# Optimization experiments

Measured on AMD Instinct MI355X. Metric: run time of the kernel, lower is better.

Reference implementation:

```python
import jax, jax.numpy as jnp
import numpy as np

B, T, D, H = 4, 2048, 1024, 16
DH = D // H  # 64
EPS = 1e-5


def _layernorm(x, g, b):
    mu = jnp.mean(x, axis=-1, keepdims=True)
    var = jnp.var(x, axis=-1, keepdims=True)
    return (x - mu) * jax.lax.rsqrt(var + EPS) * g + b


def setup_inputs() -> dict:
    key = jax.random.key(0)
    ks = jax.random.split(key, 12)
    s = 0.02
    x = jax.random.normal(ks[0], (B, T, D), dtype=jnp.float32)
    # causal mask (the repo registers tril as the eos_mask buffer)
    eos_mask = jnp.broadcast_to(jnp.tril(jnp.ones((T, T), dtype=jnp.int32)), (B, T, T))
    Wq = jax.random.normal(ks[1], (H, D, DH), dtype=jnp.float32) * s
    Wk = jax.random.normal(ks[2], (H, D, DH), dtype=jnp.float32) * s
    Wv = jax.random.normal(ks[3], (H, D, DH), dtype=jnp.float32) * s
    Wp = jax.random.normal(ks[4], (D, D), dtype=jnp.float32) * s
    bp = jnp.zeros((D,), dtype=jnp.float32)
    W1 = jax.random.normal(ks[5], (D, 4 * D), dtype=jnp.float32) * s
    b1 = jnp.zeros((4 * D,), dtype=jnp.float32)
    W2 = jax.random.normal(ks[6], (4 * D, D), dtype=jnp.float32) * s
    b2 = jnp.zeros((D,), dtype=jnp.float32)
    g1 = jnp.ones((D,), dtype=jnp.float32)
    beta1 = jnp.zeros((D,), dtype=jnp.float32)
    g2 = jnp.ones((D,), dtype=jnp.float32)
    beta2 = jnp.zeros((D,), dtype=jnp.float32)
    return dict(x=x, eos_mask=eos_mask, Wq=Wq, Wk=Wk, Wv=Wv, Wp=Wp, bp=bp,
                W1=W1, b1=b1, W2=W2, b2=b2, g1=g1, beta1=beta1, g2=g2, beta2=beta2)


def reference(x, eos_mask, Wq, Wk, Wv, Wp, bp, W1, b1, W2, b2, g1, beta1, g2, beta2):
    # x: [B,T,D]; eos_mask: [B,T,T]
    x1 = _layernorm(x, g1, beta1)
    q = jnp.einsum('btd,hdk->bhtk', x1, Wq)
    k = jnp.einsum('btd,hdk->bhtk', x1, Wk)
    v = jnp.einsum('btd,hdk->bhtk', x1, Wv)
    # NOTE: original scales by 1/sqrt(C) where C = d_model (not d_head)
    scores = jnp.einsum('bhtk,bhsk->bhts', q, k) / np.sqrt(x.shape[-1]).astype(np.float32)
    scores = jnp.where(eos_mask[:, None, :, :] == 0, jnp.float32(-jnp.inf), scores)
    wei = jax.nn.softmax(scores, axis=-1)
    attn = jnp.einsum('bhts,bhsk->bhtk', wei, v)          # [B,H,T,DH]
    attn = attn.transpose(0, 2, 1, 3).reshape(x.shape)    # concat heads -> [B,T,D]
    attn = attn @ Wp + bp
    x2 = x1 + attn
    x3 = _layernorm(x2, g2, beta2)
    mlp = jax.nn.relu(x3 @ W1 + b1) @ W2 + b2
    out = x3 + mlp
    return out
```

## Files before the change

kernel.cpp:

```cpp
#include <hip/hip_runtime.h>


#define B_ 4
#define T_ 2048
#define D_ 1024
#define H_ 16
#define DH_ 64

using u16 = unsigned short;
typedef short bf16x8 __attribute__((ext_vector_type(8)));
typedef float f32x4 __attribute__((ext_vector_type(4)));

#define GLOAD_LDS16(g, l)                                                          \
  __builtin_amdgcn_global_load_lds((const __attribute__((address_space(1))) void*)(g), \
                                   (__attribute__((address_space(3))) void*)(l), 16, 0, 0)

#define CVTPK(d, lo, hi) asm("v_cvt_pk_bf16_f32 %0, %1, %2" : "=v"(d) : "v"(lo), "v"(hi))

__device__ __forceinline__ f32x4 mfma16(bf16x8 a, bf16x8 b, f32x4 c) {
  return __builtin_amdgcn_mfma_f32_16x16x32_bf16(a, b, c, 0, 0, 0);
}

__device__ __forceinline__ u16 f2bf(float f) {
  union { float f; unsigned u; } v; v.f = f;
  unsigned r = v.u + 0x7fffu + ((v.u >> 16) & 1u);
  return (u16)(r >> 16);
}
__device__ __forceinline__ float bf2f(u16 h) {
  union { unsigned u; float f; } v; v.u = ((unsigned)h) << 16; return v.f;
}

template<typename TI>
__global__ __launch_bounds__(256)
void ln_kernel(const TI* __restrict__ x, const float* __restrict__ g,
               const float* __restrict__ be, u16* __restrict__ yb)
{
  const int row = blockIdx.x;
  const int tid = threadIdx.x;
  float v0, v1, v2, v3;
  if constexpr (sizeof(TI) == 4) {
    const float4 vx = ((const float4*)(x + (size_t)row * D_))[tid];
    v0 = vx.x; v1 = vx.y; v2 = vx.z; v3 = vx.w;
  } else {
    const ushort4 vx = ((const ushort4*)((const u16*)x + (size_t)row * D_))[tid];
    v0 = bf2f(vx.x); v1 = bf2f(vx.y); v2 = bf2f(vx.z); v3 = bf2f(vx.w);
  }
  float s  = v0 + v1 + v2 + v3;
  float s2 = v0*v0 + v1*v1 + v2*v2 + v3*v3;
#pragma unroll
  for (int m = 1; m < 64; m <<= 1) { s += __shfl_xor(s, m); s2 += __shfl_xor(s2, m); }
  __shared__ float red[8];
  const int w = tid >> 6;
  if ((tid & 63) == 0) { red[w] = s; red[4 + w] = s2; }
  __syncthreads();
  s  = red[0] + red[1] + red[2] + red[3];
  s2 = red[4] + red[5] + red[6] + red[7];
  const float mu   = s * (1.0f / D_);
  const float rstd = rsqrtf(s2 * (1.0f / D_) - mu * mu + 1e-5f);
  const float4 gg = ((const float4*)g)[tid];
  const float4 bb = ((const float4*)be)[tid];
  ushort4 pk;
  pk.x = f2bf((v0 - mu) * rstd * gg.x + bb.x);
  pk.y = f2bf((v1 - mu) * rstd * gg.y + bb.y);
  pk.z = f2bf((v2 - mu) * rstd * gg.z + bb.z);
  pk.w = f2bf((v3 - mu) * rstd * gg.w + bb.w);
  ((ushort4*)(yb + (size_t)row * D_))[tid] = pk;
}

__global__ __launch_bounds__(256)
void transpose_cvt(const float* __restrict__ in, u16* __restrict__ out, int R, int C)
{
  __shared__ float tile[32][33];
  const int c0 = blockIdx.x * 32, r0 = blockIdx.y * 32;
  const float* ip = in + (size_t)blockIdx.z * R * C;
  u16* op = out + (size_t)blockIdx.z * R * C;
  const int tx = threadIdx.x, ty = threadIdx.y;
#pragma unroll
  for (int j = 0; j < 4; ++j)
    tile[ty + j * 8][tx] = ip[(size_t)(r0 + ty + j * 8) * C + (c0 + tx)];
  __syncthreads();
#pragma unroll
  for (int j = 0; j < 4; ++j)
    op[(size_t)(c0 + ty + j * 8) * R + (r0 + tx)] = f2bf(tile[tx][ty + j * 8]);
}

#define MODE_QKV 0
#define MODE_WP 1
#define MODE_MLP1 2
#define MODE_MLP2 3

template<int MODE>
__global__ __launch_bounds__(512, 4)
void gemm128(const u16* __restrict__ A, const u16* __restrict__ Bt,
             int M, int N, int K,
             const float* __restrict__ bias, const u16* __restrict__ resid,
             float* __restrict__ outf, u16* __restrict__ outb,
             u16* __restrict__ qo, u16* __restrict__ ko, u16* __restrict__ vo)
{
  __shared__ __align__(16) u16 Ash[2][128 * 64];
  __shared__ __align__(16) u16 Bsh[2][128 * 64];
  const int t = threadIdx.x, w = t >> 6, l = t & 63, lg = l >> 4, lr = l & 15;
  const int wr = w >> 2, wc = w & 3;

  const int gx = gridDim.x;
  const int nwg = gx * gridDim.y;
  const int bid = blockIdx.y * gx + blockIdx.x;
  const int cpx = nwg >> 3;
  const int virt = (bid & 7) * cpx + (bid >> 3);
  const int bn0 = (virt % gx) * 128, bm0 = (virt / gx) * 128;

  f32x4 acc[4][2] = {};

  const int srow = t >> 3;
  const int sc16 = (t & 7) ^ (srow & 7);
  const u16* gAs = A  + (size_t)(bm0 + srow) * K + sc16 * 8;
  const u16* gBs = Bt + (size_t)(bn0 + srow) * K + sc16 * 8;

#define ISS_A(R, BUF, ko) GLOAD_LDS16(gAs + (size_t)(R) * 64 * K + (ko), &Ash[BUF][(R) * 4096 + w * 512])
#define ISS_B(R, BUF, ko) GLOAD_LDS16(gBs + (size_t)(R) * 64 * K + (ko), &Bsh[BUF][(R) * 4096 + w * 512])

  ISS_A(0, 0, 0); ISS_A(1, 0, 0); ISS_B(0, 0, 0); ISS_B(1, 0, 0);
  ISS_A(0, 1, 64); ISS_A(1, 1, 64); ISS_B(0, 1, 64); ISS_B(1, 1, 64);

  auto rdA = [&](int buf, int m, int kk) -> bf16x8 {
    const int r = wr * 64 + m * 16 + lr;
    return *(const bf16x8*)((const char*)&Ash[buf][0] + r * 128 + (((kk * 4 + lg) ^ (r & 7)) << 4));
  };
  auto rdB = [&](int buf, int n, int kk) -> bf16x8 {
    const int r = wc * 32 + n * 16 + lr;
    return *(const bf16x8*)((const char*)&Bsh[buf][0] + r * 128 + (((kk * 4 + lg) ^ (r & 7)) << 4));
  };

  const int nkt = K >> 6;
  for (int i = 0; i < nkt; ++i) {
    const int buf = i & 1;
    if (i + 1 < nkt) asm volatile("s_waitcnt vmcnt(4)" ::: "memory");
    else             asm volatile("s_waitcnt vmcnt(0)" ::: "memory");
    __builtin_amdgcn_s_barrier();
    __builtin_amdgcn_sched_barrier(0);

    bf16x8 afr[4][2], bfr[2][2];
#pragma unroll
    for (int m = 0; m < 4; ++m) { afr[m][0] = rdA(buf, m, 0); afr[m][1] = rdA(buf, m, 1); }
#pragma unroll
    for (int n = 0; n < 2; ++n) { bfr[n][0] = rdB(buf, n, 0); bfr[n][1] = rdB(buf, n, 1); }

    __builtin_amdgcn_s_setprio(1);
#pragma unroll
    for (int m = 0; m < 4; ++m)
#pragma unroll
      for (int n = 0; n < 2; ++n) {
        acc[m][n] = mfma16(afr[m][0], bfr[n][0], acc[m][n]);
        acc[m][n] = mfma16(afr[m][1], bfr[n][1], acc[m][n]);
      }
    __builtin_amdgcn_s_setprio(0);
    __builtin_amdgcn_s_barrier();
    __builtin_amdgcn_sched_barrier(0);

    if (i + 2 < nkt) {
      const size_t ko = (size_t)(i + 2) << 6;
      ISS_A(0, buf, ko); ISS_A(1, buf, ko); ISS_B(0, buf, ko); ISS_B(1, buf, ko);
    }
  }
#undef ISS_A
#undef ISS_B

#pragma unroll
  for (int m = 0; m < 4; ++m) {
#pragma unroll
    for (int n = 0; n < 2; ++n) {
#pragma unroll
      for (int r = 0; r < 4; ++r) {
        const int row = bm0 + wr * 64 + m * 16 + lg * 4 + r;
        const int col = bn0 + wc * 32 + n * 16 + lr;
        float v = acc[m][n][r];
        if constexpr (MODE == MODE_QKV) {
          const int sel = col >> 10, hh = (col >> 6) & 15, dh = col & 63;
          const int bi = row >> 11, tt = row & 2047;
          u16* dst = (sel == 0) ? qo : (sel == 1) ? ko : vo;
          dst[(((size_t)bi * H_ + hh) * T_ + tt) * DH_ + dh] = f2bf(v);
        } else if constexpr (MODE == MODE_WP) {
          v += bias[col] + bf2f(resid[(size_t)row * N + col]);
          outb[(size_t)row * N + col] = f2bf(v);
        } else if constexpr (MODE == MODE_MLP1) {
          v += bias[col];
          outb[(size_t)row * N + col] = f2bf(v > 0.f ? v : 0.f);
        } else {
          outf[(size_t)row * N + col] = v + bias[col] + bf2f(resid[(size_t)row * N + col]);
        }
      }
    }
  }
}

__global__ __launch_bounds__(256, 2)
void attn_kernel(const u16* __restrict__ q, const u16* __restrict__ k,
                 const u16* __restrict__ v, u16* __restrict__ out)
{
  __shared__ __align__(16) u16 Ks[2][4096];
  __shared__ __align__(16) u16 Vt[2][4096];
  const int t = threadIdx.x, w = t >> 6, l = t & 63, lg = l >> 4, lr = l & 15;

  const int bid = blockIdx.x;
  const int virt = (bid & 7) * 256 + (bid >> 3);
  const int bh = (virt >> 8) * 8 + (virt & 7);
  const int qt = 31 - ((virt >> 3) & 31);

  const int b = bh >> 4, h = bh & 15;
  const u16* Qp = q + (size_t)bh * T_ * DH_;
  const u16* Kp = k + (size_t)bh * T_ * DH_;
  const u16* Vp = v + (size_t)bh * T_ * DH_;

  const int qrow = qt * 64 + w * 16 + lr;
  const bf16x8 qf0 = *(const bf16x8*)&Qp[(size_t)qrow * DH_ + lg * 8];
  const bf16x8 qf1 = *(const bf16x8*)&Qp[(size_t)qrow * DH_ + 32 + lg * 8];

  const int srow = t >> 3;
  const int kcol = (((t & 7) ^ (srow & 7)) << 3);
  const int vdh0 = (t & 7) << 3;
  const u16* Kg = Kp + (size_t)srow * DH_ + kcol;
  const u16* Vg = Vp + (size_t)srow * DH_ + vdh0;

  float m_run = -1e30f, l_run = 0.f;
  f32x4 o[4] = {};
  const float SC2 = 0.03125f * 1.44269504f;
  const float THR2 = 11.5416f;

  auto writeV = [&](int buf, uint4 va, uint4 vb) {
    const u16* pa = (const u16*)&va;
    const u16* pb = (const u16*)&vb;
    char* base = (char*)&Vt[buf][0];
#pragma unroll
    for (int j = 0; j < 8; ++j) {
      const int dh = vdh0 + j;
      const int swz = (((dh & 7) ^ ((dh >> 3) & 7)) << 4);
      *(u16*)(base + (((dh << 7) + (srow << 1)) ^ swz)) = pa[j];
      *(u16*)(base + (((dh << 7) + ((32 + srow) << 1)) ^ swz)) = pb[j];
    }
  };

  GLOAD_LDS16(Kg,            &Ks[0][w * 512]);
  GLOAD_LDS16(Kg + 32 * DH_, &Ks[0][2048 + w * 512]);
  {
    uint4 v0 = *(const uint4*)Vg;
    uint4 v1 = *(const uint4*)(Vg + 32 * DH_);
    writeV(0, v0, v1);
  }
  __syncthreads();

  const int nst = qt + 1;
  for (int st = 0; st < nst; ++st) {
    const int cur = st & 1, nxt = cur ^ 1;
    uint4 vA, vB;
    const bool pf = (st + 1 < nst);
    if (pf) {
      const u16* kg = Kg + (size_t)(st + 1) * 64 * DH_;
      GLOAD_LDS16(kg,            &Ks[nxt][w * 512]);
      GLOAD_LDS16(kg + 32 * DH_, &Ks[nxt][2048 + w * 512]);
      vA = *(const uint4*)(Vg + (size_t)(st + 1) * 64 * DH_);
      vB = *(const uint4*)(Vg + (size_t)(st + 1) * 64 * DH_ + 32 * DH_);
    }

    f32x4 sa[4] = {};
    const char* kb = (const char*)&Ks[cur][0];
    __builtin_amdgcn_s_setprio(1);
#pragma unroll
    for (int n = 0; n < 4; ++n) {
      const int sr = n * 16 + lr;
      const int base = (sr << 7) + (lg << 4);
      const int swz = (sr & 7) << 4;
      const bf16x8 b0 = *(const bf16x8*)(kb + (base ^ swz));
      const bf16x8 b1 = *(const bf16x8*)(kb + ((base + 64) ^ swz));
      sa[n] = mfma16(b0, qf0, sa[n]);
      sa[n] = mfma16(b1, qf1, sa[n]);
    }
    __builtin_amdgcn_s_setprio(0);

    float sc[4][4];
    float rm = -1e30f;
#pragma unroll
    for (int n = 0; n < 4; ++n)
#pragma unroll
      for (int r = 0; r < 4; ++r) {
        float x = sa[n][r] * SC2;
        if (st == qt && (st * 64 + n * 16 + lg * 4 + r) > qrow) x = -1e30f;
        sc[n][r] = x;
        rm = fmaxf(rm, x);
      }
    rm = fmaxf(rm, __shfl_xor(rm, 16));
    rm = fmaxf(rm, __shfl_xor(rm, 32));
    const bool noresc = __all(rm <= m_run + THR2);
    if (!noresc) {
      const float mnew = fmaxf(m_run, rm);
      const float al = exp2f(m_run - mnew);
      m_run = mnew;
      l_run *= al;
      const float alr0 = __shfl(al, lg * 4 + 0);
      const float alr1 = __shfl(al, lg * 4 + 1);
      const float alr2 = __shfl(al, lg * 4 + 2);
      const float alr3 = __shfl(al, lg * 4 + 3);
#pragma unroll
      for (int n = 0; n < 4; ++n) {
        o[n][0] *= alr0; o[n][1] *= alr1; o[n][2] *= alr2; o[n][3] *= alr3;
      }
    }
    float p[4][4];
    float rs = 0.f;
#pragma unroll
    for (int n = 0; n < 4; ++n)
#pragma unroll
      for (int r = 0; r < 4; ++r) {
        p[n][r] = exp2f(sc[n][r] - m_run);
        rs += p[n][r];
      }
    rs += __shfl_xor(rs, 16);
    rs += __shfl_xor(rs, 32);
    l_run += rs;

    unsigned pk0a, pk0b, pk1a, pk1b, pk2a, pk2b, pk3a, pk3b;
    CVTPK(pk0a, p[0][0], p[0][1]); CVTPK(pk0b, p[0][2], p[0][3]);
    CVTPK(pk1a, p[1][0], p[1][1]); CVTPK(pk1b, p[1][2], p[1][3]);
    CVTPK(pk2a, p[2][0], p[2][1]); CVTPK(pk2b, p[2][2], p[2][3]);
    CVTPK(pk3a, p[3][0], p[3][1]); CVTPK(pk3b, p[3][2], p[3][3]);

    const int srcA = lr + ((l >> 4) & 1) * 32;
    const int srcB = srcA + 16;
    const bool hi = (l >> 5) & 1;
    union { uint4 u; bf16x8 v8; } f0, f1;
    {
      const unsigned xA0 = __shfl(pk0a, srcA), xA1 = __shfl(pk0b, srcA);
      const unsigned yA0 = __shfl(pk1a, srcA), yA1 = __shfl(pk1b, srcA);
      const unsigned xB0 = __shfl(pk0a, srcB), xB1 = __shfl(pk0b, srcB);
      const unsigned yB0 = __shfl(pk1a, srcB), yB1 = __shfl(pk1b, srcB);
      f0.u.x = hi ? yA0 : xA0; f0.u.y = hi ? yA1 : xA1;
      f0.u.z = hi ? yB0 : xB0; f0.u.w = hi ? yB1 : xB1;
    }
    {
      const unsigned xA0 = __shfl(pk2a, srcA), xA1 = __shfl(pk2b, srcA);
      const unsigned yA0 = __shfl(pk3a, srcA), yA1 = __shfl(pk3b, srcA);
      const unsigned xB0 = __shfl(pk2a, srcB), xB1 = __shfl(pk2b, srcB);
      const unsigned yB0 = __shfl(pk3a, srcB), yB1 = __shfl(pk3b, srcB);
      f1.u.x = hi ? yA0 : xA0; f1.u.y = hi ? yA1 : xA1;
      f1.u.z = hi ? yB0 : xB0; f1.u.w = hi ? yB1 : xB1;
    }

    const char* vbase = (const char*)&Vt[cur][0];
    __builtin_amdgcn_s_setprio(1);
#pragma unroll
    for (int ks = 0; ks < 2; ++ks) {
      const bf16x8 pa = ks ? f1.v8 : f0.v8;
#pragma unroll
      for (int n = 0; n < 4; ++n) {
        const int dh = n * 16 + lr;
        int vbyte = (dh << 7) + (ks << 6) + (lg << 4);
        vbyte ^= (((dh & 7) ^ ((dh >> 3) & 7)) << 4);
        const bf16x8 vbf = *(const bf16x8*)(vbase + vbyte);
        o[n] = mfma16(pa, vbf, o[n]);
      }
    }
    __builtin_amdgcn_s_setprio(0);

    if (pf) writeV(nxt, vA, vB);
    __syncthreads();
  }

  const size_t obase = ((size_t)b * T_) * D_ + (size_t)h * DH_;
  float li[4];
  li[0] = 1.0f / __shfl(l_run, lg * 4 + 0);
  li[1] = 1.0f / __shfl(l_run, lg * 4 + 1);
  li[2] = 1.0f / __shfl(l_run, lg * 4 + 2);
  li[3] = 1.0f / __shfl(l_run, lg * 4 + 3);
#pragma unroll
  for (int n = 0; n < 4; ++n) {
#pragma unroll
    for (int r = 0; r < 4; ++r) {
      const int qg = qt * 64 + w * 16 + lg * 4 + r;
      out[obase + (size_t)qg * D_ + n * 16 + lr] = f2bf(o[n][r] * li[r]);
    }
  }
}

extern "C" void kernel_launch(void* const* d_in, const int* in_sizes, int n_in,
                              void* d_out, int out_size, void* d_ws, size_t ws_size,
                              hipStream_t stream) {
  (void)in_sizes; (void)n_in; (void)out_size; (void)ws_size;
  const float* x   = (const float*)d_in[0];
  const float* Wq  = (const float*)d_in[2];
  const float* Wk  = (const float*)d_in[3];
  const float* Wv  = (const float*)d_in[4];
  const float* Wp  = (const float*)d_in[5];
  const float* bp  = (const float*)d_in[6];
  const float* W1  = (const float*)d_in[7];
  const float* b1  = (const float*)d_in[8];
  const float* W2  = (const float*)d_in[9];
  const float* b2  = (const float*)d_in[10];
  const float* g1  = (const float*)d_in[11];
  const float* be1 = (const float*)d_in[12];
  const float* g2  = (const float*)d_in[13];
  const float* be2 = (const float*)d_in[14];

  char* ws = (char*)d_ws;
  const size_t MB16 = 16777216;
  u16* x1b   = (u16*)(ws);
  u16* qb    = (u16*)(ws + 1 * MB16);
  u16* kb    = (u16*)(ws + 2 * MB16);
  u16* vb    = (u16*)(ws + 3 * MB16);
  u16* attnb = (u16*)(ws + 4 * MB16);
  u16* x2b   = (u16*)(ws + 5 * MB16);
  u16* hb    = (u16*)(ws + 6 * MB16);
  u16* wqkvb = (u16*)(ws + 10 * MB16);
  u16* wpb   = (u16*)(ws + 10 * MB16 + 6291456);
  u16* w1b   = (u16*)(ws + 10 * MB16 + 8388608);
  u16* w2b   = (u16*)(ws + 11 * MB16);
  u16* x3b   = qb;

  dim3 tb(32, 8, 1);
  transpose_cvt<<<dim3(2, 32, 16),  tb, 0, stream>>>(Wq, wqkvb,                    1024, 64);
  transpose_cvt<<<dim3(2, 32, 16),  tb, 0, stream>>>(Wk, wqkvb + (size_t)1048576,  1024, 64);
  transpose_cvt<<<dim3(2, 32, 16),  tb, 0, stream>>>(Wv, wqkvb + (size_t)2097152,  1024, 64);
  transpose_cvt<<<dim3(32, 32, 1),  tb, 0, stream>>>(Wp, wpb, 1024, 1024);
  transpose_cvt<<<dim3(128, 32, 1), tb, 0, stream>>>(W1, w1b, 1024, 4096);
  transpose_cvt<<<dim3(32, 128, 1), tb, 0, stream>>>(W2, w2b, 4096, 1024);

  ln_kernel<float><<<8192, 256, 0, stream>>>(x, g1, be1, x1b);

  gemm128<MODE_QKV><<<dim3(24, 64), 512, 0, stream>>>(
      x1b, wqkvb, 8192, 3072, 1024, nullptr, nullptr, nullptr, nullptr, qb, kb, vb);

  attn_kernel<<<dim3(2048), 256, 0, stream>>>(qb, kb, vb, attnb);

  gemm128<MODE_WP><<<dim3(8, 64), 512, 0, stream>>>(
      attnb, wpb, 8192, 1024, 1024, bp, x1b, nullptr, x2b, nullptr, nullptr, nullptr);

  ln_kernel<u16><<<8192, 256, 0, stream>>>(x2b, g2, be2, x3b);

  gemm128<MODE_MLP1><<<dim3(32, 64), 512, 0, stream>>>(
      x3b, w1b, 8192, 4096, 1024, b1, nullptr, nullptr, hb, nullptr, nullptr, nullptr);

  gemm128<MODE_MLP2><<<dim3(8, 64), 512, 0, stream>>>(
      hb, w2b, 8192, 1024, 4096, b2, x3b, (float*)d_out, nullptr, nullptr, nullptr, nullptr);
}
```

Measured before the change: 378.5 us.

## Add 256x256-tile GEMM with interleaved load/compute phases for QKV and MLP1

Adds a new GEMM kernel with 256x256 output tiles per 512-thread workgroup. Each K-step is split into four compute phases, and the global-to-LDS loads for the next tile are interleaved between them. The QKV and MLP1 projections now use it instead of the 128x128 kernel. The aim is better operand reuse per byte loaded and better overlap of memory with MFMA work. In exchange it uses more LDS and registers per workgroup, and launches fewer workgroups (384 for QKV, 512 for MLP1), which may leave the GPU's CUs less evenly loaded.

```diff
diff --git a/kernel.cpp b/kernel.cpp
--- a/kernel.cpp
+++ b/kernel.cpp
@@ -16,6 +16,7 @@
                                    (__attribute__((address_space(3))) void*)(l), 16, 0, 0)
 
 #define CVTPK(d, lo, hi) asm("v_cvt_pk_bf16_f32 %0, %1, %2" : "=v"(d) : "v"(lo), "v"(hi))
+#define BARSB() do { __builtin_amdgcn_s_barrier(); __builtin_amdgcn_sched_barrier(0); } while (0)
 
 __device__ __forceinline__ f32x4 mfma16(bf16x8 a, bf16x8 b, f32x4 c) {
   return __builtin_amdgcn_mfma_f32_16x16x32_bf16(a, b, c, 0, 0, 0);
@@ -90,6 +91,159 @@
 #define MODE_MLP2 3
 
 template<int MODE>
+__global__ __launch_bounds__(512, 2)
+void gemm256v2(const u16* __restrict__ A, const u16* __restrict__ Bt,
+               int M, int N, int K,
+               const float* __restrict__ bias, const u16* __restrict__ resid,
+               float* __restrict__ outf, u16* __restrict__ outb,
+               u16* __restrict__ qo, u16* __restrict__ ko, u16* __restrict__ vo)
+{
+  __shared__ __align__(16) u16 Ash[2][256 * 64];
+  __shared__ __align__(16) u16 Bsh[2][256 * 64];
+  const int t = threadIdx.x, w = t >> 6, l = t & 63, lg = l >> 4, lr = l & 15;
+  const int wr = w >> 2, wc = w & 3;
+
+  const int gx = gridDim.x;
+  const int nwg = gx * gridDim.y;
+  const int bid = blockIdx.y * gx + blockIdx.x;
+  const int cpx = nwg >> 3;
+  const int virt = (bid & 7) * cpx + (bid >> 3);
+  const int bn0 = (virt % gx) * 256, bm0 = (virt / gx) * 256;
+
+  f32x4 acc[8][4] = {};
+
+  const int srow = t >> 3;
+  const int sc16 = (t & 7) ^ (srow & 7);
+  const u16* gAs = A  + (size_t)(bm0 + srow) * K + sc16 * 8;
+  const u16* gBs = Bt + (size_t)(bn0 + srow) * K + sc16 * 8;
+
+#define ISS2_A(R, BUF, ko) GLOAD_LDS16(gAs + (size_t)(R) * 64 * K + (ko), &Ash[BUF][(R) * 4096 + w * 512])
+#define ISS2_B(R, BUF, ko) GLOAD_LDS16(gBs + (size_t)(R) * 64 * K + (ko), &Bsh[BUF][(R) * 4096 + w * 512])
+
+  const int nkt = K >> 6;
+  ISS2_A(0, 0, 0); ISS2_A(1, 0, 0); ISS2_A(2, 0, 0); ISS2_A(3, 0, 0);
+  ISS2_B(0, 0, 0); ISS2_B(1, 0, 0); ISS2_B(2, 0, 0); ISS2_B(3, 0, 0);
+  if (nkt > 1) {
+    ISS2_A(0, 1, 64); ISS2_A(1, 1, 64);
+    asm volatile("s_waitcnt vmcnt(2)" ::: "memory");
+  } else {
+    asm volatile("s_waitcnt vmcnt(0)" ::: "memory");
+  }
+  BARSB();
+
+  auto rdA = [&](int buf, int m) -> bf16x8 {
+    const int r = wr * 128 + m * 16 + lr;
+    return *(const bf16x8*)((const char*)&Ash[buf][0] + r * 128 + (((0 + lg) ^ (r & 7)) << 4));
+  };
+  auto rdA1 = [&](int buf, int m) -> bf16x8 {
+    const int r = wr * 128 + m * 16 + lr;
+    return *(const bf16x8*)((const char*)&Ash[buf][0] + r * 128 + (((4 + lg) ^ (r & 7)) << 4));
+  };
+  auto rdB0 = [&](int buf, int n) -> bf16x8 {
+    const int r = wc * 64 + n * 16 + lr;
+    return *(const bf16x8*)((const char*)&Bsh[buf][0] + r * 128 + (((0 + lg) ^ (r & 7)) << 4));
+  };
+  auto rdB1 = [&](int buf, int n) -> bf16x8 {
+    const int r = wc * 64 + n * 16 + lr;
+    return *(const bf16x8*)((const char*)&Bsh[buf][0] + r * 128 + (((4 + lg) ^ (r & 7)) << 4));
+  };
+
+  bf16x8 afr[4][2], bfr[4][2];
+
+  for (int i = 0; i < nkt; ++i) {
+    const int buf = i & 1, nb = buf ^ 1;
+    const size_t k1 = (size_t)(i + 1) << 6, k2 = (size_t)(i + 2) << 6;
+    const bool n1 = (i + 1 < nkt), n2 = (i + 2 < nkt);
+
+#pragma unroll
+    for (int m = 0; m < 4; ++m) { afr[m][0] = rdA(buf, m); afr[m][1] = rdA1(buf, m); }
+#pragma unroll
+    for (int n = 0; n < 2; ++n) { bfr[n][0] = rdB0(buf, n); bfr[n][1] = rdB1(buf, n); }
+    if (n1) { ISS2_A(2, nb, k1); ISS2_A(3, nb, k1); }
+    BARSB();
+    __builtin_amdgcn_s_setprio(1);
+#pragma unroll
+    for (int m = 0; m < 4; ++m)
+#pragma unroll
+      for (int n = 0; n < 2; ++n) {
+        acc[m][n] = mfma16(afr[m][0], bfr[n][0], acc[m][n]);
+        acc[m][n] = mfma16(afr[m][1], bfr[n][1], acc[m][n]);
+      }
+    __builtin_amdgcn_s_setprio(0);
+    BARSB();
+
+#pragma unroll
+    for (int n = 2; n < 4; ++n) { bfr[n][0] = rdB0(buf, n); bfr[n][1] = rdB1(buf, n); }
+    if (n1) { ISS2_B(0, nb, k1); ISS2_B(1, nb, k1); }
+    BARSB();
+    __builtin_amdgcn_s_setprio(1);
+#pragma unroll
+    for (int m = 0; m < 4; ++m)
+#pragma unroll
+      for (int n = 2; n < 4; ++n) {
+        acc[m][n] = mfma16(afr[m][0], bfr[n][0], acc[m][n]);
+        acc[m][n] = mfma16(afr[m][1], bfr[n][1], acc[m][n]);
+      }
+    __builtin_amdgcn_s_setprio(0);
+    BARSB();
+
+#pragma unroll
+    for (int m = 0; m < 4; ++m) { afr[m][0] = rdA(buf, 4 + m); afr[m][1] = rdA1(buf, 4 + m); }
+    if (n1) { ISS2_B(2, nb, k1); ISS2_B(3, nb, k1); }
+    BARSB();
+    __builtin_amdgcn_s_setprio(1);
+#pragma unroll
+    for (int m = 0; m < 4; ++m)
+#pragma unroll
+      for (int n = 0; n < 2; ++n) {
+        acc[4 + m][n] = mfma16(afr[m][0], bfr[n][0], acc[4 + m][n]);
+        acc[4 + m][n] = mfma16(afr[m][1], bfr[n][1], acc[4 + m][n]);
+      }
+    __builtin_amdgcn_s_setprio(0);
+    BARSB();
+
+    if (n2) { ISS2_A(0, buf, k2); ISS2_A(1, buf, k2); }
+    BARSB();
+    __builtin_amdgcn_s_setprio(1);
+#pragma unroll
+    for (int m = 0; m < 4; ++m)
+#pragma unroll
+      for (int n = 2; n < 4; ++n) {
+        acc[4 + m][n] = mfma16(afr[m][0], bfr[n][0], acc[4 + m][n]);
+        acc[4 + m][n] = mfma16(afr[m][1], bfr[n][1], acc[4 + m][n]);
+      }
+    __builtin_amdgcn_s_setprio(0);
+    if (n2) asm volatile("s_waitcnt vmcnt(2)" ::: "memory");
+    else    asm volatile("s_waitcnt vmcnt(0)" ::: "memory");
+    BARSB();
+  }
+#undef ISS2_A
+#undef ISS2_B
+
+#pragma unroll
+  for (int m = 0; m < 8; ++m) {
+#pragma unroll
+    for (int n = 0; n < 4; ++n) {
+#pragma unroll
+      for (int r = 0; r < 4; ++r) {
+        const int row = bm0 + wr * 128 + m * 16 + lg * 4 + r;
+        const int col = bn0 + wc * 64 + n * 16 + lr;
+        float v = acc[m][n][r];
+        if constexpr (MODE == MODE_QKV) {
+          const int sel = col >> 10, hh = (col >> 6) & 15, dh = col & 63;
+          const int bi = row >> 11, tt = row & 2047;
+          u16* dst = (sel == 0) ? qo : (sel == 1) ? ko : vo;
+          dst[(((size_t)bi * H_ + hh) * T_ + tt) * DH_ + dh] = f2bf(v);
+        } else if constexpr (MODE == MODE_MLP1) {
+          v += bias[col];
+          outb[(size_t)row * N + col] = f2bf(v > 0.f ? v : 0.f);
+        }
+      }
+    }
+  }
+}
+
+template<int MODE>
 __global__ __launch_bounds__(512, 4)
 void gemm128(const u16* __restrict__ A, const u16* __restrict__ Bt,
              int M, int N, int K,
@@ -136,8 +290,7 @@
     const int buf = i & 1;
     if (i + 1 < nkt) asm volatile("s_waitcnt vmcnt(4)" ::: "memory");
     else             asm volatile("s_waitcnt vmcnt(0)" ::: "memory");
-    __builtin_amdgcn_s_barrier();
-    __builtin_amdgcn_sched_barrier(0);
+    BARSB();
 
     bf16x8 afr[4][2], bfr[2][2];
 #pragma unroll
@@ -154,8 +307,7 @@
         acc[m][n] = mfma16(afr[m][1], bfr[n][1], acc[m][n]);
       }
     __builtin_amdgcn_s_setprio(0);
-    __builtin_amdgcn_s_barrier();
-    __builtin_amdgcn_sched_barrier(0);
+    BARSB();
 
     if (i + 2 < nkt) {
       const size_t ko = (size_t)(i + 2) << 6;
@@ -174,18 +326,10 @@
         const int row = bm0 + wr * 64 + m * 16 + lg * 4 + r;
         const int col = bn0 + wc * 32 + n * 16 + lr;
         float v = acc[m][n][r];
-        if constexpr (MODE == MODE_QKV) {
-          const int sel = col >> 10, hh = (col >> 6) & 15, dh = col & 63;
-          const int bi = row >> 11, tt = row & 2047;
-          u16* dst = (sel == 0) ? qo : (sel == 1) ? ko : vo;
-          dst[(((size_t)bi * H_ + hh) * T_ + tt) * DH_ + dh] = f2bf(v);
-        } else if constexpr (MODE == MODE_WP) {
+        if constexpr (MODE == MODE_WP) {
           v += bias[col] + bf2f(resid[(size_t)row * N + col]);
           outb[(size_t)row * N + col] = f2bf(v);
-        } else if constexpr (MODE == MODE_MLP1) {
-          v += bias[col];
-          outb[(size_t)row * N + col] = f2bf(v > 0.f ? v : 0.f);
-        } else {
+        } else if constexpr (MODE == MODE_MLP2) {
           outf[(size_t)row * N + col] = v + bias[col] + bf2f(resid[(size_t)row * N + col]);
         }
       }
@@ -424,7 +568,7 @@
 
   ln_kernel<float><<<8192, 256, 0, stream>>>(x, g1, be1, x1b);
 
-  gemm128<MODE_QKV><<<dim3(24, 64), 512, 0, stream>>>(
+  gemm256v2<MODE_QKV><<<dim3(12, 32), 512, 0, stream>>>(
       x1b, wqkvb, 8192, 3072, 1024, nullptr, nullptr, nullptr, nullptr, qb, kb, vb);
 
   attn_kernel<<<dim3(2048), 256, 0, stream>>>(qb, kb, vb, attnb);
@@ -434,7 +578,7 @@
 
   ln_kernel<u16><<<8192, 256, 0, stream>>>(x2b, g2, be2, x3b);
 
-  gemm128<MODE_MLP1><<<dim3(32, 64), 512, 0, stream>>>(
+  gemm256v2<MODE_MLP1><<<dim3(16, 32), 512, 0, stream>>>(
       x3b, w1b, 8192, 4096, 1024, b1, nullptr, nullptr, hb, nullptr, nullptr, nullptr);
 
   gemm128<MODE_MLP2><<<dim3(8, 64), 512, 0, stream>>>(
```

Result: faster. 370.7 us (-2.1%).
